# Optimization experiments

Hardware: AMD Instinct MI355X
Metric: run time of the kernel (lower is better)

The kernel has to match this reference:

```python
import jax, jax.numpy as jnp
import numpy as np

DIM_IN = 256  # dim_in_d * dim_in_length


def _quad_feats(h):
    # h: [B, d] -> [B, d + d*(d+1)//2] : concat(h, triu(outer(h, h)))
    d = h.shape[1]
    iu, ju = jnp.triu_indices(d)  # includes diagonal, matching torch.triu_indices
    outer = h[:, :, None] * h[:, None, :]          # [B, d, d]
    hsq = outer[:, iu, ju]                         # [B, d*(d+1)//2]
    return jnp.concatenate([h, hsq], axis=-1)


def setup_inputs() -> dict:
    key = jax.random.key(0)
    ks = jax.random.split(key, 7)
    d = DIM_IN
    q = d + (d * d + d) // 2  # 33152
    scale = 0.01  # keep activations bounded through quadratic features
    return {
        "x": jax.random.normal(ks[0], (4096, 16, 16), dtype=jnp.float32),
        "W0": jax.random.normal(ks[1], (256, q), dtype=jnp.float32) * scale,
        "b0": jax.random.normal(ks[2], (256,), dtype=jnp.float32) * scale,
        "W1": jax.random.normal(ks[3], (256, q), dtype=jnp.float32) * scale,
        "b1": jax.random.normal(ks[4], (256,), dtype=jnp.float32) * scale,
        "W2": jax.random.normal(ks[5], (10, q), dtype=jnp.float32) * scale,
        "b2": jax.random.normal(ks[6], (10,), dtype=jnp.float32) * scale,
    }


def reference(x, W0, b0, W1, b1, W2, b2):
    B = x.shape[0]
    h = x.reshape(B, -1)  # flatten: [B, dim_in_d*dim_in_length]
    for W, b in ((W0, b0), (W1, b1), (W2, b2)):
        z = _quad_feats(h)                  # [B, d + d(d+1)/2]
        h = jnp.einsum('bq,oq->bo', z, W) + b
    return h
```

## Files before the change

### kernel.cpp

```cpp
#include <hip/hip_runtime.h>
#include <stdint.h>

#define Q_IN 33152
#define NTILES 1160
#define TPC 145

typedef _Float16 half8 __attribute__((ext_vector_type(8)));
typedef float floatx4 __attribute__((ext_vector_type(4)));
typedef uint32_t uint4v __attribute__((ext_vector_type(4)));

__global__ void build_tab(uint32_t* tab) {
  int T = blockIdx.x * 256 + threadIdx.x;
  if (T >= NTILES) return;
  int kch = T / TPC, tt = T % TPC;
  int i0, jb;
  if (tt == 0) { i0 = -1; jb = 32 * kch; }
  else {
    int Q = kch * 144 + (tt - 1);
    int grp = Q >> 5, s = Q & 31;
    int g = 0, base = 0;
    for (; g < 8; ++g) { int cnt = 8 - g; if (grp < base + cnt) break; base += cnt; }
    int jt = grp - base;
    i0 = 32 * g + s;
    jb = 32 * (g + jt);
  }
  tab[T] = (((uint32_t)(uint16_t)(short)i0) << 16) | (uint32_t)(uint16_t)jb;
}

__global__ void convert_w(const float* __restrict__ W, _Float16* __restrict__ Wt,
                          const uint32_t* __restrict__ tab, int NTT, int Oreal) {
  int tid = blockIdx.x * 256 + threadIdx.x;
  if (tid >= NTILES * NTT * 64) return;
  int l = tid & 63;
  int nt = (tid >> 6) % NTT;
  int T = tid / (64 * NTT);
  int o = nt * 16 + (l & 15);
  int koff = (l >> 4) * 8;
  half8 v;
#pragma unroll
  for (int t = 0; t < 8; ++t) v[t] = (_Float16)0.f;
  if (o < Oreal) {
    uint32_t e = tab[T];
    int i0 = (short)(e >> 16);
    int jb = (int)(e & 0xFFFFu);
    const float* row = W + (size_t)o * Q_IN;
    if (i0 < 0) {
#pragma unroll
      for (int t = 0; t < 8; ++t) v[t] = (_Float16)row[jb + koff + t];
    } else {
      int qb = 256 + i0 * 256 - (i0 * (i0 - 1)) / 2 - i0;
#pragma unroll
      for (int t = 0; t < 8; ++t) {
        int j = jb + koff + t;
        if (j >= i0) v[t] = (_Float16)row[qb + j];
      }
    }
  }
  *(half8*)(Wt + (size_t)(T * NTT + nt) * 512 + l * 8) = v;
}

__global__ void reduce_h(const float* __restrict__ part, const float* __restrict__ bias,
                         float* __restrict__ h) {
  int t = blockIdx.x * 256 + threadIdx.x;
  float4 acc = *(const float4*)(bias + ((t & 63) << 2));
#pragma unroll
  for (int k = 0; k < 8; ++k) {
    float4 p = *(const float4*)(part + (size_t)k * 1048576 + t * 4);
    acc.x += p.x; acc.y += p.y; acc.z += p.z; acc.w += p.w;
  }
  *(float4*)(h + t * 4) = acc;
}

__global__ void reduce_out(const float* __restrict__ part2, const float* __restrict__ b2,
                           float* __restrict__ out) {
  int t = blockIdx.x * 256 + threadIdx.x;
  if (t >= 40960) return;
  int b = t / 10, o = t - b * 10;
  float acc = b2[o];
#pragma unroll
  for (int k = 0; k < 8; ++k) acc += part2[(size_t)k * 65536 + b * 16 + o];
  out[t] = acc;
}

__device__ inline floatx4 mfma16(half8 a, half8 b, floatx4 c) {
  return __builtin_amdgcn_mfma_f32_16x16x32_f16(a, b, c, 0, 0, 0);
}

__device__ inline half8 splat_mul_lo(half8 a, uint32_t s) {
  uint4v av = __builtin_bit_cast(uint4v, a), r;
#pragma unroll
  for (int k = 0; k < 4; ++k)
    asm("v_pk_mul_f16 %0, %1, %2 op_sel:[0,0] op_sel_hi:[1,0]"
        : "=v"(r[k]) : "v"(av[k]), "v"(s));
  return __builtin_bit_cast(half8, r);
}
__device__ inline half8 splat_mul_hi(half8 a, uint32_t s) {
  uint4v av = __builtin_bit_cast(uint4v, a), r;
#pragma unroll
  for (int k = 0; k < 4; ++k)
    asm("v_pk_mul_f16 %0, %1, %2 op_sel:[0,1] op_sel_hi:[1,1]"
        : "=v"(r[k]) : "v"(av[k]), "v"(s));
  return __builtin_bit_cast(half8, r);
}

__global__ __launch_bounds__(512, 1) void qgemm_main(
    const float* __restrict__ hIn, const _Float16* __restrict__ Wt,
    float* __restrict__ part, const uint32_t* __restrict__ gtab) {
  __shared__ _Float16 hT[128 * 256];

  const int tid = threadIdx.x;
  const int l = tid & 63;
  const int wid = tid >> 6;
  const int kch = blockIdx.x & 7;
  const int rb = blockIdx.x >> 3;
  const int tbase = kch * TPC;

  const char* gb = (const char*)Wt + (size_t)tbase * 16384;
  const uint32_t lo = (uint32_t)(wid * 2048 + l * 16);

  half8 blin0 = *(const half8*)(gb + lo);
  half8 blin1 = *(const half8*)(gb + (lo + 1024));
  const char* gq = gb + 16384;
  half8 gA[4][2], gB[4][2];
#pragma unroll
  for (int sp = 0; sp < 4; ++sp) {
    gA[sp][0] = *(const half8*)(gq + (lo + sp * 16384u));
    gA[sp][1] = *(const half8*)(gq + (lo + sp * 16384u + 1024u));
  }
#pragma unroll
  for (int sp = 0; sp < 4; ++sp) {
    gB[sp][0] = *(const half8*)(gq + (lo + (4 + sp) * 16384u));
    gB[sp][1] = *(const half8*)(gq + (lo + (4 + sp) * 16384u + 1024u));
  }

  {
    int r = tid >> 2, sg = tid & 3;
    const float* src = hIn + (size_t)(rb * 128 + r) * 256 + sg * 64;
    char* dst = (char*)hT + r * 512;
    int xo = (r & 7) << 4;
#pragma unroll
    for (int oc = 0; oc < 8; ++oc) {
      float4 f0 = *(const float4*)(src + oc * 8);
      float4 f1 = *(const float4*)(src + oc * 8 + 4);
      half8 hv;
      hv[0] = (_Float16)f0.x; hv[1] = (_Float16)f0.y;
      hv[2] = (_Float16)f0.z; hv[3] = (_Float16)f0.w;
      hv[4] = (_Float16)f1.x; hv[5] = (_Float16)f1.y;
      hv[6] = (_Float16)f1.z; hv[7] = (_Float16)f1.w;
      *(half8*)(dst + ((sg * 128 + oc * 16) ^ xo)) = hv;
    }
  }
  __syncthreads();

  floatx4 acc[8][2];
#pragma unroll
  for (int mt = 0; mt < 8; ++mt)
#pragma unroll
    for (int nt = 0; nt < 2; ++nt)
#pragma unroll
      for (int rg = 0; rg < 4; ++rg) acc[mt][nt][rg] = 0.f;

  int rowb[8];
#pragma unroll
  for (int mt = 0; mt < 8; ++mt) rowb[mt] = (mt * 16 + (l & 15)) * 512;
  const int xorb = (l & 7) << 4;
  const int koffA = (l >> 4) * 16;
  const char* hTb = (const char*)hT;

  half8 a[8];
  int prevjb;

  {
    uint32_t e0 = gtab[tbase];
    int jb = (int)(e0 & 0xFFFFu);
#pragma unroll
    for (int mt = 0; mt < 8; ++mt)
      a[mt] = *(const half8*)(hTb + rowb[mt] + ((jb * 2 + koffA) ^ xorb));
#pragma unroll
    for (int mt = 0; mt < 8; ++mt) {
      acc[mt][0] = mfma16(a[mt], blin0, acc[mt][0]);
      acc[mt][1] = mfma16(a[mt], blin1, acc[mt][1]);
    }
    prevjb = jb;
  }

  uint32_t e = gtab[tbase + 1];
  for (int b = 0; b < 18; ++b) {
    uint32_t enext = (b < 17) ? gtab[tbase + 1 + (b + 1) * 8] : 0u;
    int i0b = (int)(e >> 16);
    int jb = (int)(e & 0xFFFFu);
    uint4v scu[8];
#pragma unroll
    for (int mt = 0; mt < 8; ++mt)
      scu[mt] = *(const uint4v*)(hTb + rowb[mt] + ((i0b * 2) ^ xorb));
    if (jb != prevjb) {
      prevjb = jb;
#pragma unroll
      for (int mt = 0; mt < 8; ++mt)
        a[mt] = *(const half8*)(hTb + rowb[mt] + ((jb * 2 + koffA) ^ xorb));
    }
    const char* gqn = gq + 131072;

#pragma unroll
    for (int sp = 0; sp < 4; ++sp) {
#pragma unroll
      for (int mt = 0; mt < 8; ++mt) {
        half8 as_ = (sp & 1) ? splat_mul_hi(a[mt], scu[mt][sp >> 1])
                             : splat_mul_lo(a[mt], scu[mt][sp >> 1]);
        acc[mt][0] = mfma16(as_, gA[sp][0], acc[mt][0]);
        acc[mt][1] = mfma16(as_, gA[sp][1], acc[mt][1]);
      }
    }
    if (b < 17) {
#pragma unroll
      for (int sp = 0; sp < 4; ++sp) {
        gA[sp][0] = *(const half8*)(gqn + (lo + sp * 16384u));
        gA[sp][1] = *(const half8*)(gqn + (lo + sp * 16384u + 1024u));
      }
    }
#pragma unroll
    for (int sp = 0; sp < 4; ++sp) {
#pragma unroll
      for (int mt = 0; mt < 8; ++mt) {
        half8 as_ = (sp & 1) ? splat_mul_hi(a[mt], scu[mt][2 + (sp >> 1)])
                             : splat_mul_lo(a[mt], scu[mt][2 + (sp >> 1)]);
        acc[mt][0] = mfma16(as_, gB[sp][0], acc[mt][0]);
        acc[mt][1] = mfma16(as_, gB[sp][1], acc[mt][1]);
      }
    }
    if (b < 17) {
#pragma unroll
      for (int sp = 0; sp < 4; ++sp) {
        gB[sp][0] = *(const half8*)(gqn + (lo + (4 + sp) * 16384u));
        gB[sp][1] = *(const half8*)(gqn + (lo + (4 + sp) * 16384u + 1024u));
      }
    }
    gq = gqn;
    e = enext;
  }

  float* op = part + (size_t)kch * 1048576;
  const int r0 = rb * 128;
  const int c0 = wid * 32;
#pragma unroll
  for (int mt = 0; mt < 8; ++mt) {
    int rbase = r0 + mt * 16 + (l >> 4) * 4;
#pragma unroll
    for (int nt = 0; nt < 2; ++nt) {
      int c = c0 + nt * 16 + (l & 15);
#pragma unroll
      for (int rg = 0; rg < 4; ++rg)
        op[(size_t)(rbase + rg) * 256 + c] = acc[mt][nt][rg];
    }
  }
}

__global__ __launch_bounds__(512, 2) void qgemm_small(
    const float* __restrict__ hIn, const _Float16* __restrict__ Wt,
    float* __restrict__ part2, const uint32_t* __restrict__ gtab) {
  __shared__ _Float16 hT[128 * 256];
  const int tid = threadIdx.x;
  const int l = tid & 63;
  const int wid = tid >> 6;
  const int kch = blockIdx.x & 7;
  const int rb = blockIdx.x >> 3;
  const int tbase = kch * TPC;

  {
    int r = tid >> 2, sg = tid & 3;
    const float* src = hIn + (size_t)(rb * 128 + r) * 256 + sg * 64;
    char* dst = (char*)hT + r * 512;
    int xo = (r & 7) << 4;
#pragma unroll
    for (int oc = 0; oc < 8; ++oc) {
      float4 f0 = *(const float4*)(src + oc * 8);
      float4 f1 = *(const float4*)(src + oc * 8 + 4);
      half8 hv;
      hv[0] = (_Float16)f0.x; hv[1] = (_Float16)f0.y;
      hv[2] = (_Float16)f0.z; hv[3] = (_Float16)f0.w;
      hv[4] = (_Float16)f1.x; hv[5] = (_Float16)f1.y;
      hv[6] = (_Float16)f1.z; hv[7] = (_Float16)f1.w;
      *(half8*)(dst + ((sg * 128 + oc * 16) ^ xo)) = hv;
    }
  }
  __syncthreads();

  floatx4 acc;
#pragma unroll
  for (int rg = 0; rg < 4; ++rg) acc[rg] = 0.f;

  const int rowb = (wid * 16 + (l & 15)) * 512;
  const int xorb = (l & 7) << 4;
  const int koffA = (l >> 4) * 16;
  const char* hTb = (const char*)hT;

  half8 a, sc;
  int prevjb;

  {
    uint32_t e0 = gtab[tbase];
    int jb = (int)(e0 & 0xFFFFu);
    a = *(const half8*)(hTb + rowb + ((jb * 2 + koffA) ^ xorb));
    half8 b = *(const half8*)(Wt + (size_t)tbase * 512 + l * 8);
    acc = mfma16(a, b, acc);
    prevjb = jb;
  }

  for (int u8 = 0; u8 < 18; ++u8) {
    uint32_t e = gtab[tbase + 1 + u8 * 8];
    int i0b = (int)(e >> 16);
    int jb = (int)(e & 0xFFFFu);
    const int ttb = tbase + 1 + u8 * 8;
    half8 bq[8];
#pragma unroll
    for (int s = 0; s < 8; ++s)
      bq[s] = *(const half8*)(Wt + (size_t)(ttb + s) * 512 + l * 8);
    if (jb != prevjb) {
      prevjb = jb;
      a = *(const half8*)(hTb + rowb + ((jb * 2 + koffA) ^ xorb));
    }
    sc = *(const half8*)(hTb + rowb + ((i0b * 2) ^ xorb));
#pragma unroll
    for (int s = 0; s < 8; ++s) {
      _Float16 sv = sc[s];
      half8 sb = {sv, sv, sv, sv, sv, sv, sv, sv};
      acc = mfma16(a * sb, bq[s], acc);
    }
  }

  float* op = part2 + (size_t)kch * 65536;
  const int r0 = rb * 128 + wid * 16 + (l >> 4) * 4;
  const int c = l & 15;
#pragma unroll
  for (int rg = 0; rg < 4; ++rg)
    op[(size_t)(r0 + rg) * 16 + c] = acc[rg];
}

extern "C" void kernel_launch(void* const* d_in, const int* in_sizes, int n_in,
                              void* d_out, int out_size, void* d_ws, size_t ws_size,
                              hipStream_t stream) {
  const float* x = (const float*)d_in[0];
  const float* W0 = (const float*)d_in[1];
  const float* b0 = (const float*)d_in[2];
  const float* W1 = (const float*)d_in[3];
  const float* b1 = (const float*)d_in[4];
  const float* W2 = (const float*)d_in[5];
  const float* b2 = (const float*)d_in[6];
  float* out = (float*)d_out;

  char* ws = (char*)d_ws;
  float* h1 = (float*)ws;
  float* h2 = (float*)(ws + (4u << 20));
  _Float16* Wt = (_Float16*)(ws + (8u << 20));
  uint32_t* tab = (uint32_t*)(ws + (8u << 20) + 19005440u);
  float* part = (float*)(ws + (28u << 20));
  float* part2 = part;

  build_tab<<<(NTILES + 255) / 256, 256, 0, stream>>>(tab);

  convert_w<<<(NTILES * 16 * 64) / 256, 256, 0, stream>>>(W0, Wt, tab, 16, 256);
  qgemm_main<<<256, 512, 0, stream>>>(x, Wt, part, tab);
  reduce_h<<<1024, 256, 0, stream>>>(part, b0, h1);
  convert_w<<<(NTILES * 16 * 64) / 256, 256, 0, stream>>>(W1, Wt, tab, 16, 256);
  qgemm_main<<<256, 512, 0, stream>>>(h1, Wt, part, tab);
  reduce_h<<<1024, 256, 0, stream>>>(part, b1, h2);
  convert_w<<<(NTILES * 1 * 64 + 255) / 256, 256, 0, stream>>>(W2, Wt, tab, 1, 10);
  qgemm_small<<<256, 512, 0, stream>>>(h2, Wt, part2, tab);
  reduce_out<<<160, 256, 0, stream>>>(part2, b2, out);
}
```

Baseline: 237.7 us.

## Retile qgemm_main warps to 2x4 grid with finer-grained weight prefetch pipeline

Changes each warp's output tile from 128 rows by 32 columns to 64 rows by 64 columns, using a 2x4 warp grid. Each splatted A fragment now feeds four MFMAs instead of two, which halves the per-warp splat multiplies and LDS reads of h. Weight fragments are double-buffered in two half-size register sets (G0/G1) that are refilled after each quarter of the block, so loads overlap compute more evenly. Each warp now loads twice as many weight bytes per tile, which raises global/L2 traffic for weights and may change register pressure.

```diff
diff --git a/kernel.cpp b/kernel.cpp
--- a/kernel.cpp
+++ b/kernel.cpp
@@ -111,27 +111,38 @@
   const int tid = threadIdx.x;
   const int l = tid & 63;
   const int wid = tid >> 6;
+  const int wm = wid >> 2;
+  const int wn = wid & 3;
   const int kch = blockIdx.x & 7;
   const int rb = blockIdx.x >> 3;
   const int tbase = kch * TPC;
 
   const char* gb = (const char*)Wt + (size_t)tbase * 16384;
-  const uint32_t lo = (uint32_t)(wid * 2048 + l * 16);
-
-  half8 blin0 = *(const half8*)(gb + lo);
-  half8 blin1 = *(const half8*)(gb + (lo + 1024));
   const char* gq = gb + 16384;
-  half8 gA[4][2], gB[4][2];
-#pragma unroll
-  for (int sp = 0; sp < 4; ++sp) {
-    gA[sp][0] = *(const half8*)(gq + (lo + sp * 16384u));
-    gA[sp][1] = *(const half8*)(gq + (lo + sp * 16384u + 1024u));
-  }
-#pragma unroll
-  for (int sp = 0; sp < 4; ++sp) {
-    gB[sp][0] = *(const half8*)(gq + (lo + (4 + sp) * 16384u));
-    gB[sp][1] = *(const half8*)(gq + (lo + (4 + sp) * 16384u + 1024u));
-  }
+  const uint32_t lo = (uint32_t)(wn * 4096 + l * 16);
+
+  half8 blin[4];
+#pragma unroll
+  for (int j = 0; j < 4; ++j)
+    blin[j] = *(const half8*)(gb + (lo + j * 1024u));
+
+  half8 G0[2][4], G1[2][4];
+  auto issueG0 = [&](uint32_t qt) {
+#pragma unroll
+    for (int t2 = 0; t2 < 2; ++t2)
+#pragma unroll
+      for (int j = 0; j < 4; ++j)
+        G0[t2][j] = *(const half8*)(gq + (lo + (qt + t2) * 16384u + j * 1024u));
+  };
+  auto issueG1 = [&](uint32_t qt) {
+#pragma unroll
+    for (int t2 = 0; t2 < 2; ++t2)
+#pragma unroll
+      for (int j = 0; j < 4; ++j)
+        G1[t2][j] = *(const half8*)(gq + (lo + (qt + t2) * 16384u + j * 1024u));
+  };
+  issueG0(0);
+  issueG1(2);
 
   {
     int r = tid >> 2, sg = tid & 3;
@@ -152,102 +163,88 @@
   }
   __syncthreads();
 
-  floatx4 acc[8][2];
-#pragma unroll
-  for (int mt = 0; mt < 8; ++mt)
-#pragma unroll
-    for (int nt = 0; nt < 2; ++nt)
+  floatx4 acc[4][4];
+#pragma unroll
+  for (int mt = 0; mt < 4; ++mt)
+#pragma unroll
+    for (int nt = 0; nt < 4; ++nt)
 #pragma unroll
       for (int rg = 0; rg < 4; ++rg) acc[mt][nt][rg] = 0.f;
 
-  int rowb[8];
-#pragma unroll
-  for (int mt = 0; mt < 8; ++mt) rowb[mt] = (mt * 16 + (l & 15)) * 512;
+  int rowb[4];
+#pragma unroll
+  for (int mt = 0; mt < 4; ++mt)
+    rowb[mt] = (wm * 64 + mt * 16 + (l & 15)) * 512;
   const int xorb = (l & 7) << 4;
   const int koffA = (l >> 4) * 16;
   const char* hTb = (const char*)hT;
 
-  half8 a[8];
+  half8 a[4];
+  uint4v scu[4];
   int prevjb;
+
+  auto loadA = [&](int jb) {
+#pragma unroll
+    for (int mt = 0; mt < 4; ++mt)
+      a[mt] = *(const half8*)(hTb + rowb[mt] + ((jb * 2 + koffA) ^ xorb));
+  };
+  auto consumeG0 = [&](const int t2, const int s) {
+#pragma unroll
+    for (int mt = 0; mt < 4; ++mt) {
+      uint32_t sd = scu[mt][s >> 1];
+      half8 as_ = (s & 1) ? splat_mul_hi(a[mt], sd) : splat_mul_lo(a[mt], sd);
+#pragma unroll
+      for (int j = 0; j < 4; ++j)
+        acc[mt][j] = mfma16(as_, G0[t2][j], acc[mt][j]);
+    }
+  };
+  auto consumeG1 = [&](const int t2, const int s) {
+#pragma unroll
+    for (int mt = 0; mt < 4; ++mt) {
+      uint32_t sd = scu[mt][s >> 1];
+      half8 as_ = (s & 1) ? splat_mul_hi(a[mt], sd) : splat_mul_lo(a[mt], sd);
+#pragma unroll
+      for (int j = 0; j < 4; ++j)
+        acc[mt][j] = mfma16(as_, G1[t2][j], acc[mt][j]);
+    }
+  };
 
   {
     uint32_t e0 = gtab[tbase];
     int jb = (int)(e0 & 0xFFFFu);
-#pragma unroll
-    for (int mt = 0; mt < 8; ++mt)
-      a[mt] = *(const half8*)(hTb + rowb[mt] + ((jb * 2 + koffA) ^ xorb));
-#pragma unroll
-    for (int mt = 0; mt < 8; ++mt) {
-      acc[mt][0] = mfma16(a[mt], blin0, acc[mt][0]);
-      acc[mt][1] = mfma16(a[mt], blin1, acc[mt][1]);
-    }
+    loadA(jb);
+#pragma unroll
+    for (int mt = 0; mt < 4; ++mt)
+#pragma unroll
+      for (int j = 0; j < 4; ++j)
+        acc[mt][j] = mfma16(a[mt], blin[j], acc[mt][j]);
     prevjb = jb;
   }
 
-  uint32_t e = gtab[tbase + 1];
-  for (int b = 0; b < 18; ++b) {
-    uint32_t enext = (b < 17) ? gtab[tbase + 1 + (b + 1) * 8] : 0u;
+  uint32_t qt = 0;
+  for (int blk = 0; blk < 18; ++blk) {
+    uint32_t e = gtab[tbase + 1 + blk * 8];
     int i0b = (int)(e >> 16);
     int jb = (int)(e & 0xFFFFu);
-    uint4v scu[8];
-#pragma unroll
-    for (int mt = 0; mt < 8; ++mt)
+#pragma unroll
+    for (int mt = 0; mt < 4; ++mt)
       scu[mt] = *(const uint4v*)(hTb + rowb[mt] + ((i0b * 2) ^ xorb));
-    if (jb != prevjb) {
-      prevjb = jb;
-#pragma unroll
-      for (int mt = 0; mt < 8; ++mt)
-        a[mt] = *(const half8*)(hTb + rowb[mt] + ((jb * 2 + koffA) ^ xorb));
-    }
-    const char* gqn = gq + 131072;
-
-#pragma unroll
-    for (int sp = 0; sp < 4; ++sp) {
-#pragma unroll
-      for (int mt = 0; mt < 8; ++mt) {
-        half8 as_ = (sp & 1) ? splat_mul_hi(a[mt], scu[mt][sp >> 1])
-                             : splat_mul_lo(a[mt], scu[mt][sp >> 1]);
-        acc[mt][0] = mfma16(as_, gA[sp][0], acc[mt][0]);
-        acc[mt][1] = mfma16(as_, gA[sp][1], acc[mt][1]);
-      }
-    }
-    if (b < 17) {
-#pragma unroll
-      for (int sp = 0; sp < 4; ++sp) {
-        gA[sp][0] = *(const half8*)(gqn + (lo + sp * 16384u));
-        gA[sp][1] = *(const half8*)(gqn + (lo + sp * 16384u + 1024u));
-      }
-    }
-#pragma unroll
-    for (int sp = 0; sp < 4; ++sp) {
-#pragma unroll
-      for (int mt = 0; mt < 8; ++mt) {
-        half8 as_ = (sp & 1) ? splat_mul_hi(a[mt], scu[mt][2 + (sp >> 1)])
-                             : splat_mul_lo(a[mt], scu[mt][2 + (sp >> 1)]);
-        acc[mt][0] = mfma16(as_, gB[sp][0], acc[mt][0]);
-        acc[mt][1] = mfma16(as_, gB[sp][1], acc[mt][1]);
-      }
-    }
-    if (b < 17) {
-#pragma unroll
-      for (int sp = 0; sp < 4; ++sp) {
-        gB[sp][0] = *(const half8*)(gqn + (lo + (4 + sp) * 16384u));
-        gB[sp][1] = *(const half8*)(gqn + (lo + (4 + sp) * 16384u + 1024u));
-      }
-    }
-    gq = gqn;
-    e = enext;
+    if (jb != prevjb) { prevjb = jb; loadA(jb); }
+
+    consumeG0(0, 0); consumeG0(1, 1); issueG0(qt + 4);
+    consumeG1(0, 2); consumeG1(1, 3); issueG1(qt + 6);
+    consumeG0(0, 4); consumeG0(1, 5); if (blk < 17) issueG0(qt + 8);
+    consumeG1(0, 6); consumeG1(1, 7); if (blk < 17) issueG1(qt + 10);
+    qt += 8;
   }
 
   float* op = part + (size_t)kch * 1048576;
-  const int r0 = rb * 128;
-  const int c0 = wid * 32;
-#pragma unroll
-  for (int mt = 0; mt < 8; ++mt) {
-    int rbase = r0 + mt * 16 + (l >> 4) * 4;
-#pragma unroll
-    for (int nt = 0; nt < 2; ++nt) {
-      int c = c0 + nt * 16 + (l & 15);
+#pragma unroll
+  for (int mt = 0; mt < 4; ++mt) {
+    int rbase = rb * 128 + wm * 64 + mt * 16 + (l >> 4) * 4;
+#pragma unroll
+    for (int nt = 0; nt < 4; ++nt) {
+      int c = wn * 64 + nt * 16 + (l & 15);
 #pragma unroll
       for (int rg = 0; rg < 4; ++rg)
         op[(size_t)(rbase + rg) * 256 + c] = acc[mt][nt][rg];
```

Result: slower. 249.1 us (+4.8%).

## Store hidden activations as swizzled fp16 and split small GEMM K-range

Applied to the files above, without the earlier changes.

The reduction kernels now write intermediate activations directly as fp16 in the XOR-swizzled LDS layout. Later GEMMs can then stage them with direct global-to-LDS loads instead of loading fp32 and converting per block. Separately, the final small GEMM doubles its grid by splitting each K-chunk's loop into two halves, with the final reduction summing 16 partials instead of 8. This cuts activation bandwidth and conversion work and raises parallelism in the last layer, at the cost of an extra partial-buffer pass.

```diff
diff --git a/kernel.cpp b/kernel.cpp
--- a/kernel.cpp
+++ b/kernel.cpp
@@ -59,16 +59,19 @@
   *(half8*)(Wt + (size_t)(T * NTT + nt) * 512 + l * 8) = v;
 }
 
-__global__ void reduce_h(const float* __restrict__ part, const float* __restrict__ bias,
-                         float* __restrict__ h) {
+__global__ void reduce_h16(const float* __restrict__ part, const float* __restrict__ bias,
+                           char* __restrict__ h) {
   int t = blockIdx.x * 256 + threadIdx.x;
-  float4 acc = *(const float4*)(bias + ((t & 63) << 2));
+  int row = t >> 6, c4 = (t & 63) << 2;
+  float4 acc = *(const float4*)(bias + c4);
 #pragma unroll
   for (int k = 0; k < 8; ++k) {
     float4 p = *(const float4*)(part + (size_t)k * 1048576 + t * 4);
     acc.x += p.x; acc.y += p.y; acc.z += p.z; acc.w += p.w;
   }
-  *(float4*)(h + t * 4) = acc;
+  _Float16 hv[4] = {(_Float16)acc.x, (_Float16)acc.y, (_Float16)acc.z, (_Float16)acc.w};
+  *(uint64_t*)(h + (size_t)row * 512 + ((c4 * 2) ^ ((row & 7) << 4))) =
+      *(const uint64_t*)hv;
 }
 
 __global__ void reduce_out(const float* __restrict__ part2, const float* __restrict__ b2,
@@ -78,12 +81,18 @@
   int b = t / 10, o = t - b * 10;
   float acc = b2[o];
 #pragma unroll
-  for (int k = 0; k < 8; ++k) acc += part2[(size_t)k * 65536 + b * 16 + o];
+  for (int k = 0; k < 16; ++k) acc += part2[(size_t)k * 65536 + b * 16 + o];
   out[t] = acc;
 }
 
 __device__ inline floatx4 mfma16(half8 a, half8 b, floatx4 c) {
   return __builtin_amdgcn_mfma_f32_16x16x32_f16(a, b, c, 0, 0, 0);
+}
+
+__device__ inline void gload_lds16(const void* g, void* l) {
+  __builtin_amdgcn_global_load_lds(
+      (const __attribute__((address_space(1))) uint32_t*)g,
+      (__attribute__((address_space(3))) uint32_t*)l, 16, 0, 0);
 }
 
 __device__ inline half8 splat_mul_lo(half8 a, uint32_t s) {
@@ -103,8 +112,34 @@
   return __builtin_bit_cast(half8, r);
 }
 
+__device__ inline void stage_f32(_Float16* hT, const float* src0, int rb, int tid) {
+  int r = tid >> 2, sg = tid & 3;
+  const float* src = src0 + (size_t)(rb * 128 + r) * 256 + sg * 64;
+  char* dst = (char*)hT + r * 512;
+  int xo = (r & 7) << 4;
+#pragma unroll
+  for (int oc = 0; oc < 8; ++oc) {
+    float4 f0 = *(const float4*)(src + oc * 8);
+    float4 f1 = *(const float4*)(src + oc * 8 + 4);
+    half8 hv;
+    hv[0] = (_Float16)f0.x; hv[1] = (_Float16)f0.y;
+    hv[2] = (_Float16)f0.z; hv[3] = (_Float16)f0.w;
+    hv[4] = (_Float16)f1.x; hv[5] = (_Float16)f1.y;
+    hv[6] = (_Float16)f1.z; hv[7] = (_Float16)f1.w;
+    *(half8*)(dst + ((sg * 128 + oc * 16) ^ xo)) = hv;
+  }
+}
+
+__device__ inline void stage_f16(_Float16* hT, const char* h, int rb, int tid) {
+#pragma unroll
+  for (int it = 0; it < 8; ++it)
+    gload_lds16(h + (size_t)rb * 65536 + it * 8192 + tid * 16,
+                (char*)hT + it * 8192 + tid * 16);
+}
+
+template <int F16IN>
 __global__ __launch_bounds__(512, 1) void qgemm_main(
-    const float* __restrict__ hIn, const _Float16* __restrict__ Wt,
+    const void* __restrict__ hIn, const _Float16* __restrict__ Wt,
     float* __restrict__ part, const uint32_t* __restrict__ gtab) {
   __shared__ _Float16 hT[128 * 256];
 
@@ -133,23 +168,8 @@
     gB[sp][1] = *(const half8*)(gq + (lo + (4 + sp) * 16384u + 1024u));
   }
 
-  {
-    int r = tid >> 2, sg = tid & 3;
-    const float* src = hIn + (size_t)(rb * 128 + r) * 256 + sg * 64;
-    char* dst = (char*)hT + r * 512;
-    int xo = (r & 7) << 4;
-#pragma unroll
-    for (int oc = 0; oc < 8; ++oc) {
-      float4 f0 = *(const float4*)(src + oc * 8);
-      float4 f1 = *(const float4*)(src + oc * 8 + 4);
-      half8 hv;
-      hv[0] = (_Float16)f0.x; hv[1] = (_Float16)f0.y;
-      hv[2] = (_Float16)f0.z; hv[3] = (_Float16)f0.w;
-      hv[4] = (_Float16)f1.x; hv[5] = (_Float16)f1.y;
-      hv[6] = (_Float16)f1.z; hv[7] = (_Float16)f1.w;
-      *(half8*)(dst + ((sg * 128 + oc * 16) ^ xo)) = hv;
-    }
-  }
+  if (F16IN) stage_f16(hT, (const char*)hIn, rb, tid);
+  else       stage_f32(hT, (const float*)hIn, rb, tid);
   __syncthreads();
 
   floatx4 acc[8][2];
@@ -256,33 +276,19 @@
 }
 
 __global__ __launch_bounds__(512, 2) void qgemm_small(
-    const float* __restrict__ hIn, const _Float16* __restrict__ Wt,
+    const void* __restrict__ hIn, const _Float16* __restrict__ Wt,
     float* __restrict__ part2, const uint32_t* __restrict__ gtab) {
   __shared__ _Float16 hT[128 * 256];
   const int tid = threadIdx.x;
   const int l = tid & 63;
   const int wid = tid >> 6;
   const int kch = blockIdx.x & 7;
-  const int rb = blockIdx.x >> 3;
+  const int rest = blockIdx.x >> 3;
+  const int wk = rest & 1;
+  const int rb = rest >> 1;
   const int tbase = kch * TPC;
 
-  {
-    int r = tid >> 2, sg = tid & 3;
-    const float* src = hIn + (size_t)(rb * 128 + r) * 256 + sg * 64;
-    char* dst = (char*)hT + r * 512;
-    int xo = (r & 7) << 4;
-#pragma unroll
-    for (int oc = 0; oc < 8; ++oc) {
-      float4 f0 = *(const float4*)(src + oc * 8);
-      float4 f1 = *(const float4*)(src + oc * 8 + 4);
-      half8 hv;
-      hv[0] = (_Float16)f0.x; hv[1] = (_Float16)f0.y;
-      hv[2] = (_Float16)f0.z; hv[3] = (_Float16)f0.w;
-      hv[4] = (_Float16)f1.x; hv[5] = (_Float16)f1.y;
-      hv[6] = (_Float16)f1.z; hv[7] = (_Float16)f1.w;
-      *(half8*)(dst + ((sg * 128 + oc * 16) ^ xo)) = hv;
-    }
-  }
+  stage_f16(hT, (const char*)hIn, rb, tid);
   __syncthreads();
 
   floatx4 acc;
@@ -295,9 +301,9 @@
   const char* hTb = (const char*)hT;
 
   half8 a, sc;
-  int prevjb;
-
-  {
+  int prevjb = -1;
+
+  if (wk == 0) {
     uint32_t e0 = gtab[tbase];
     int jb = (int)(e0 & 0xFFFFu);
     a = *(const half8*)(hTb + rowb + ((jb * 2 + koffA) ^ xorb));
@@ -306,7 +312,7 @@
     prevjb = jb;
   }
 
-  for (int u8 = 0; u8 < 18; ++u8) {
+  for (int u8 = wk * 9; u8 < wk * 9 + 9; ++u8) {
     uint32_t e = gtab[tbase + 1 + u8 * 8];
     int i0b = (int)(e >> 16);
     int jb = (int)(e & 0xFFFFu);
@@ -328,7 +334,7 @@
     }
   }
 
-  float* op = part2 + (size_t)kch * 65536;
+  float* op = part2 + (size_t)(kch * 2 + wk) * 65536;
   const int r0 = rb * 128 + wid * 16 + (l >> 4) * 4;
   const int c = l & 15;
 #pragma unroll
@@ -349,8 +355,8 @@
   float* out = (float*)d_out;
 
   char* ws = (char*)d_ws;
-  float* h1 = (float*)ws;
-  float* h2 = (float*)(ws + (4u << 20));
+  char* h1 = ws;
+  char* h2 = ws + (4u << 20);
   _Float16* Wt = (_Float16*)(ws + (8u << 20));
   uint32_t* tab = (uint32_t*)(ws + (8u << 20) + 19005440u);
   float* part = (float*)(ws + (28u << 20));
@@ -359,12 +365,12 @@
   build_tab<<<(NTILES + 255) / 256, 256, 0, stream>>>(tab);
 
   convert_w<<<(NTILES * 16 * 64) / 256, 256, 0, stream>>>(W0, Wt, tab, 16, 256);
-  qgemm_main<<<256, 512, 0, stream>>>(x, Wt, part, tab);
-  reduce_h<<<1024, 256, 0, stream>>>(part, b0, h1);
+  qgemm_main<0><<<256, 512, 0, stream>>>(x, Wt, part, tab);
+  reduce_h16<<<1024, 256, 0, stream>>>(part, b0, h1);
   convert_w<<<(NTILES * 16 * 64) / 256, 256, 0, stream>>>(W1, Wt, tab, 16, 256);
-  qgemm_main<<<256, 512, 0, stream>>>(h1, Wt, part, tab);
-  reduce_h<<<1024, 256, 0, stream>>>(part, b1, h2);
+  qgemm_main<1><<<256, 512, 0, stream>>>(h1, Wt, part, tab);
+  reduce_h16<<<1024, 256, 0, stream>>>(part, b1, h2);
   convert_w<<<(NTILES * 1 * 64 + 255) / 256, 256, 0, stream>>>(W2, Wt, tab, 1, 10);
-  qgemm_small<<<256, 512, 0, stream>>>(h2, Wt, part2, tab);
+  qgemm_small<<<512, 512, 0, stream>>>(h2, Wt, part2, tab);
   reduce_out<<<160, 256, 0, stream>>>(part2, b2, out);
 }
```

Result: faster. 230.6 us (-3.0%).
